# Performance work log

Hardware: AMD Instinct MI355X
Metric: run time of the kernel (lower is better)

## Reference

```python
import jax, jax.numpy as jnp
import numpy as np

N_SAMPLES = 9
N_FEATURES = 8
GRID_DIM = 200
H, W = 512, 512


def _corner_shifts():
    # same ordering as the torch module: i (x) outer, j (y), k (z) inner
    return jnp.array([[i, j, k] for i in (0, 1) for j in (0, 1) for k in (0, 1)], dtype=jnp.int32)


def setup_inputs() -> dict:
    key = jax.random.key(0)
    k1, k2, k3, k4 = jax.random.split(key, 4)
    b = 1
    vpoints = jax.random.uniform(k1, (b, H * W, 3), jnp.float32, 0.0, float(GRID_DIM))
    veye = jax.random.uniform(k2, (b, 3), jnp.float32, -float(GRID_DIM), 0.0)
    depth = jax.random.uniform(k3, (b, H, W), jnp.float32)
    grid = jax.random.normal(k4, (GRID_DIM, GRID_DIM, GRID_DIM, N_FEATURES), jnp.float32)
    empty_value = jnp.zeros((N_FEATURES,), jnp.float32)
    return {"vpoints": vpoints, "veye": veye, "depth": depth, "grid": grid, "empty_value": empty_value}


def _forward(vpoints, veye, depth, grid, empty_value):
    b, h, w = depth.shape
    # --- create_canonical_view: n_samples points along each viewing ray, centered on vpoints ---
    dirs = vpoints - veye[:, None, :]                                   # (b, n, 3)
    dirs = dirs / jnp.linalg.norm(dirs, axis=-1, keepdims=True)
    offs = jnp.arange(N_SAMPLES, dtype=vpoints.dtype) - (N_SAMPLES // 2)
    cv = vpoints[:, :, None, :] + offs[None, None, :, None] * dirs[:, :, None, :]  # (b, n, s, 3)
    points_normalized = cv - (jnp.floor(cv) + 0.5)

    pts = cv.reshape(-1, 3)  # b == 1 (original squeezes the batch dim); N = n*s
    xs, ys, zs, nf = grid.shape
    valid = ((pts[:, 0] >= 0) & (pts[:, 0] < xs)
             & (pts[:, 1] >= 0) & (pts[:, 1] < ys)
             & (pts[:, 2] >= 0) & (pts[:, 2] < zs))

    # replication-pad volume by 1 voxel; coords shifted by +1 into padded frame
    gp = jnp.pad(grid, ((1, 1), (1, 1), (1, 1), (0, 0)), mode="edge")
    p = jnp.where(valid[:, None], pts, 0.0) + 1.0   # invalid points mapped to a safe in-bounds index
    fl = jnp.floor(p)
    df = p - fl                                      # (N, 3) fractional offsets
    base = fl.astype(jnp.int32)
    idx = base[:, None, :] + _corner_shifts()[None]  # (N, 8, 3)

    corners = gp[idx[..., 0], idx[..., 1], idx[..., 2], :]  # (N, 8, nf) gather

    # trilinear weights, ordering matches corner shift ordering (4i + 2j + k)
    wx = jnp.stack([1.0 - df[:, 0], df[:, 0]], axis=1)
    wy = jnp.stack([1.0 - df[:, 1], df[:, 1]], axis=1)
    wz = jnp.stack([1.0 - df[:, 2], df[:, 2]], axis=1)
    wgt = (wx[:, :, None, None] * wy[:, None, :, None] * wz[:, None, None, :]).reshape(-1, 8)

    interp = jnp.einsum("nc,ncf->nf", wgt, corners)              # (N, nf)
    feats = jnp.where(valid[:, None], interp, empty_value[None, :])

    values = feats.reshape(b, h, w, N_SAMPLES * N_FEATURES)
    values = jnp.transpose(values, (0, 3, 1, 2))                 # (b, s*nf, h, w)
    return values, points_normalized, dirs


def reference(vpoints, veye, depth, grid, empty_value):
    return _forward(vpoints, veye, depth, grid, empty_value)
```

## Files before the change

kernel.cpp:

```cpp
#include <hip/hip_runtime.h>

#define HW (512 * 512)
#define GD 200
#define NS 9
#define NF 8
#define NPB 64
#define BT (NPB * NS)

__global__ __launch_bounds__(BT, 5) void fusion_gather_kernel(
    const float* __restrict__ vpoints,
    const float* __restrict__ veye,
    const float* __restrict__ grid,
    const float* __restrict__ empty_value,
    float* __restrict__ out_values,
    float* __restrict__ out_pn,
    float* __restrict__ out_dirs)
{
    __shared__ float pnbuf[NPB * NS * 3];
    __shared__ float dirbuf[NPB * 3];

    int tid = threadIdx.x;
    int s = tid >> 6;
    int i = tid & 63;
    int n0 = blockIdx.x * NPB;
    int n = n0 + i;

    float px = vpoints[n * 3 + 0];
    float py = vpoints[n * 3 + 1];
    float pz = vpoints[n * 3 + 2];
    float ex = veye[0], ey = veye[1], ez = veye[2];

    float dx = px - ex, dy = py - ey, dz = pz - ez;
    float inv = 1.0f / sqrtf(dx * dx + dy * dy + dz * dz);
    dx *= inv; dy *= inv; dz *= inv;

    if (s == 4) {
        dirbuf[i * 3 + 0] = dx;
        dirbuf[i * 3 + 1] = dy;
        dirbuf[i * 3 + 2] = dz;
    }

    float off = (float)(s - NS / 2);
    float cx = px + off * dx;
    float cy = py + off * dy;
    float cz = pz + off * dz;

    pnbuf[i * 27 + s * 3 + 0] = cx - (floorf(cx) + 0.5f);
    pnbuf[i * 27 + s * 3 + 1] = cy - (floorf(cy) + 0.5f);
    pnbuf[i * 27 + s * 3 + 2] = cz - (floorf(cz) + 0.5f);

    bool valid = (cx >= 0.0f) && (cx < (float)GD) &&
                 (cy >= 0.0f) && (cy < (float)GD) &&
                 (cz >= 0.0f) && (cz < (float)GD);

    float p0 = cx + 1.0f, p1 = cy + 1.0f, p2 = cz + 1.0f;
    float f0 = floorf(p0), f1 = floorf(p1), f2 = floorf(p2);
    float d0 = p0 - f0, d1 = p1 - f1, d2 = p2 - f2;
    int bx = (int)f0, by = (int)f1, bz = (int)f2;
    int X0 = min(max(bx - 1, 0), GD - 1), X1 = min(max(bx, 0), GD - 1);
    int Y0 = min(max(by - 1, 0), GD - 1), Y1 = min(max(by, 0), GD - 1);
    int Z0 = min(max(bz - 1, 0), GD - 1), Z1 = min(max(bz, 0), GD - 1);

    const float4* __restrict__ g4 = (const float4*)grid;

    int col[4];
    col[0] = (X0 * GD + Y0) * GD;
    col[1] = (X0 * GD + Y1) * GD;
    col[2] = (X1 * GD + Y0) * GD;
    col[3] = (X1 * GD + Y1) * GD;

    float4 c[16];
#pragma unroll
    for (int q = 0; q < 4; ++q) {
        c[q * 4 + 0] = g4[(size_t)(col[q] + Z0) * 2 + 0];
        c[q * 4 + 1] = g4[(size_t)(col[q] + Z0) * 2 + 1];
        c[q * 4 + 2] = g4[(size_t)(col[q] + Z1) * 2 + 0];
        c[q * 4 + 3] = g4[(size_t)(col[q] + Z1) * 2 + 1];
    }

    float wx0 = 1.0f - d0, wx1 = d0;
    float wy0 = 1.0f - d1, wy1 = d1;
    float wz0 = 1.0f - d2, wz1 = d2;
    float wq[4];
    wq[0] = wx0 * wy0; wq[1] = wx0 * wy1; wq[2] = wx1 * wy0; wq[3] = wx1 * wy1;

    float acc[NF];
#pragma unroll
    for (int f = 0; f < NF; ++f) acc[f] = 0.0f;

#pragma unroll
    for (int q = 0; q < 4; ++q) {
        float w0 = wq[q] * wz0, w1 = wq[q] * wz1;
        acc[0] += w0 * c[q * 4 + 0].x + w1 * c[q * 4 + 2].x;
        acc[1] += w0 * c[q * 4 + 0].y + w1 * c[q * 4 + 2].y;
        acc[2] += w0 * c[q * 4 + 0].z + w1 * c[q * 4 + 2].z;
        acc[3] += w0 * c[q * 4 + 0].w + w1 * c[q * 4 + 2].w;
        acc[4] += w0 * c[q * 4 + 1].x + w1 * c[q * 4 + 3].x;
        acc[5] += w0 * c[q * 4 + 1].y + w1 * c[q * 4 + 3].y;
        acc[6] += w0 * c[q * 4 + 1].z + w1 * c[q * 4 + 3].z;
        acc[7] += w0 * c[q * 4 + 1].w + w1 * c[q * 4 + 3].w;
    }

    float ev[NF];
#pragma unroll
    for (int f = 0; f < NF; ++f) ev[f] = empty_value[f];

#pragma unroll
    for (int f = 0; f < NF; ++f)
        __builtin_nontemporal_store(valid ? acc[f] : ev[f],
                                    &out_values[(size_t)(s * NF + f) * HW + n]);

    __syncthreads();

    const size_t pn_base = (size_t)n0 * (NS * 3);
#pragma unroll
    for (int k = 0; k < 3; ++k) {
        int idx = tid + k * BT;
        __builtin_nontemporal_store(pnbuf[idx], &out_pn[pn_base + idx]);
    }
    if (tid < NPB * 3)
        __builtin_nontemporal_store(dirbuf[tid], &out_dirs[(size_t)n0 * 3 + tid]);
}

extern "C" void kernel_launch(void* const* d_in, const int* in_sizes, int n_in,
                              void* d_out, int out_size, void* d_ws, size_t ws_size,
                              hipStream_t stream) {
    const float* vpoints = (const float*)d_in[0];
    const float* veye = (const float*)d_in[1];
    const float* grid = (const float*)d_in[3];
    const float* empty_value = (const float*)d_in[4];

    float* out = (float*)d_out;
    float* out_values = out;
    float* out_pn = out + (size_t)NS * NF * HW;
    float* out_dirs = out_pn + (size_t)HW * NS * 3;

    dim3 block(BT);
    dim3 grid_dim(HW / NPB);
    hipLaunchKernelGGL(fusion_gather_kernel, grid_dim, block, 0, stream,
                       vpoints, veye, grid, empty_value,
                       out_values, out_pn, out_dirs);
}
```

Baseline: 172.2 us.

## Remap threads so each ray's samples are adjacent and stage outputs through shared memory

Threads are reassigned so the 9 samples of one ray are consecutive lanes (r = tid/9, s = tid%9), which makes neighbouring lanes hit nearby grid voxels for better gather locality. vpoints are staged through shared memory. The feature outputs go into a padded shared buffer and are written back as coalesced rows. The occupancy hint in launch_bounds is dropped. This adds about 18KB of shared memory per block, which may lower occupancy, and adds an integer division.

Result: faster. 158.1 us (median of 2 runs) (-8.2%).

```diff
diff --git a/kernel.cpp b/kernel.cpp
--- a/kernel.cpp
+++ b/kernel.cpp
@@ -7,7 +7,7 @@
 #define NPB 64
 #define BT (NPB * NS)
 
-__global__ __launch_bounds__(BT, 5) void fusion_gather_kernel(
+__global__ __launch_bounds__(BT) void fusion_gather_kernel(
     const float* __restrict__ vpoints,
     const float* __restrict__ veye,
     const float* __restrict__ grid,
@@ -16,28 +16,33 @@
     float* __restrict__ out_pn,
     float* __restrict__ out_dirs)
 {
+    __shared__ float vp[NPB * 3];
     __shared__ float pnbuf[NPB * NS * 3];
     __shared__ float dirbuf[NPB * 3];
+    __shared__ float vbuf[NS * NF * 65];
 
     int tid = threadIdx.x;
-    int s = tid >> 6;
-    int i = tid & 63;
     int n0 = blockIdx.x * NPB;
-    int n = n0 + i;
 
-    float px = vpoints[n * 3 + 0];
-    float py = vpoints[n * 3 + 1];
-    float pz = vpoints[n * 3 + 2];
+    if (tid < NPB * 3) vp[tid] = vpoints[(size_t)n0 * 3 + tid];
+    __syncthreads();
+
+    int r = tid / NS;
+    int s = tid - r * NS;
+
+    float px = vp[r * 3 + 0];
+    float py = vp[r * 3 + 1];
+    float pz = vp[r * 3 + 2];
     float ex = veye[0], ey = veye[1], ez = veye[2];
 
     float dx = px - ex, dy = py - ey, dz = pz - ez;
     float inv = 1.0f / sqrtf(dx * dx + dy * dy + dz * dz);
     dx *= inv; dy *= inv; dz *= inv;
 
-    if (s == 4) {
-        dirbuf[i * 3 + 0] = dx;
-        dirbuf[i * 3 + 1] = dy;
-        dirbuf[i * 3 + 2] = dz;
+    if (s == 0) {
+        dirbuf[r * 3 + 0] = dx;
+        dirbuf[r * 3 + 1] = dy;
+        dirbuf[r * 3 + 2] = dz;
     }
 
     float off = (float)(s - NS / 2);
@@ -45,9 +50,9 @@
     float cy = py + off * dy;
     float cz = pz + off * dz;
 
-    pnbuf[i * 27 + s * 3 + 0] = cx - (floorf(cx) + 0.5f);
-    pnbuf[i * 27 + s * 3 + 1] = cy - (floorf(cy) + 0.5f);
-    pnbuf[i * 27 + s * 3 + 2] = cz - (floorf(cz) + 0.5f);
+    pnbuf[r * 27 + s * 3 + 0] = cx - (floorf(cx) + 0.5f);
+    pnbuf[r * 27 + s * 3 + 1] = cy - (floorf(cy) + 0.5f);
+    pnbuf[r * 27 + s * 3 + 2] = cz - (floorf(cz) + 0.5f);
 
     bool valid = (cx >= 0.0f) && (cx < (float)GD) &&
                  (cy >= 0.0f) && (cy < (float)GD) &&
@@ -107,11 +112,20 @@
 
 #pragma unroll
     for (int f = 0; f < NF; ++f)
-        __builtin_nontemporal_store(valid ? acc[f] : ev[f],
-                                    &out_values[(size_t)(s * NF + f) * HW + n]);
+        vbuf[(s * NF + f) * 65 + r] = valid ? acc[f] : ev[f];
 
     __syncthreads();
 
+    {
+        int col_ = tid & 63;
+        int w = tid >> 6;
+#pragma unroll
+        for (int k = 0; k < 8; ++k) {
+            int row = w + k * NS;
+            __builtin_nontemporal_store(vbuf[row * 65 + col_],
+                                        &out_values[(size_t)row * HW + n0 + col_]);
+        }
+    }
     const size_t pn_base = (size_t)n0 * (NS * 3);
 #pragma unroll
     for (int k = 0; k < 3; ++k) {
```

## Map each ray's nine samples onto adjacent lanes and stage value writes through shared memory

Applied to the files above, without the earlier changes.

Threads are remapped so the nine samples of a ray sit on consecutive lanes of a wave (7 rays per wave, 28 rays per 256-thread block) instead of one sample index per wave. Interpolated values are staged in a padded shared buffer and written out cooperatively per feature row. The goal is to improve locality of the grid gathers, since samples of one ray touch nearby voxels, while keeping the output writes contiguous. In exchange, one lane per wave sits idle, each block writes only 28-float row segments, and there is extra LDS traffic plus a partial tail block.

Result: no change. 171.4 us (-0.5%).

```diff
diff --git a/kernel.cpp b/kernel.cpp
--- a/kernel.cpp
+++ b/kernel.cpp
@@ -4,10 +4,11 @@
 #define GD 200
 #define NS 9
 #define NF 8
-#define NPB 64
-#define BT (NPB * NS)
+#define NPB 28
+#define BT 256
+#define P 29
 
-__global__ __launch_bounds__(BT, 5) void fusion_gather_kernel(
+__global__ __launch_bounds__(BT) void fusion_gather_kernel(
     const float* __restrict__ vpoints,
     const float* __restrict__ veye,
     const float* __restrict__ grid,
@@ -16,109 +17,127 @@
     float* __restrict__ out_pn,
     float* __restrict__ out_dirs)
 {
-    __shared__ float pnbuf[NPB * NS * 3];
+    __shared__ float vbuf[NS * NF * P];
+    __shared__ float pnbuf[NPB * 27];
     __shared__ float dirbuf[NPB * 3];
 
     int tid = threadIdx.x;
-    int s = tid >> 6;
-    int i = tid & 63;
+    int w = tid >> 6;
+    int l = tid & 63;
     int n0 = blockIdx.x * NPB;
-    int n = n0 + i;
+    int nvalid = min(NPB, HW - n0);
 
-    float px = vpoints[n * 3 + 0];
-    float py = vpoints[n * 3 + 1];
-    float pz = vpoints[n * 3 + 2];
-    float ex = veye[0], ey = veye[1], ez = veye[2];
+    if (l < 63) {
+        int r = l / 9;
+        int s = l - r * 9;
+        int lr = w * 7 + r;
+        if (lr < nvalid) {
+            int n = n0 + lr;
 
-    float dx = px - ex, dy = py - ey, dz = pz - ez;
-    float inv = 1.0f / sqrtf(dx * dx + dy * dy + dz * dz);
-    dx *= inv; dy *= inv; dz *= inv;
+            float px = vpoints[n * 3 + 0];
+            float py = vpoints[n * 3 + 1];
+            float pz = vpoints[n * 3 + 2];
+            float ex = veye[0], ey = veye[1], ez = veye[2];
 
-    if (s == 4) {
-        dirbuf[i * 3 + 0] = dx;
-        dirbuf[i * 3 + 1] = dy;
-        dirbuf[i * 3 + 2] = dz;
-    }
+            float dx = px - ex, dy = py - ey, dz = pz - ez;
+            float inv = 1.0f / sqrtf(dx * dx + dy * dy + dz * dz);
+            dx *= inv; dy *= inv; dz *= inv;
 
-    float off = (float)(s - NS / 2);
-    float cx = px + off * dx;
-    float cy = py + off * dy;
-    float cz = pz + off * dz;
+            if (s == 0) {
+                dirbuf[lr * 3 + 0] = dx;
+                dirbuf[lr * 3 + 1] = dy;
+                dirbuf[lr * 3 + 2] = dz;
+            }
 
-    pnbuf[i * 27 + s * 3 + 0] = cx - (floorf(cx) + 0.5f);
-    pnbuf[i * 27 + s * 3 + 1] = cy - (floorf(cy) + 0.5f);
-    pnbuf[i * 27 + s * 3 + 2] = cz - (floorf(cz) + 0.5f);
+            float off = (float)(s - NS / 2);
+            float cx = px + off * dx;
+            float cy = py + off * dy;
+            float cz = pz + off * dz;
 
-    bool valid = (cx >= 0.0f) && (cx < (float)GD) &&
-                 (cy >= 0.0f) && (cy < (float)GD) &&
-                 (cz >= 0.0f) && (cz < (float)GD);
+            pnbuf[lr * 27 + s * 3 + 0] = cx - (floorf(cx) + 0.5f);
+            pnbuf[lr * 27 + s * 3 + 1] = cy - (floorf(cy) + 0.5f);
+            pnbuf[lr * 27 + s * 3 + 2] = cz - (floorf(cz) + 0.5f);
 
-    float p0 = cx + 1.0f, p1 = cy + 1.0f, p2 = cz + 1.0f;
-    float f0 = floorf(p0), f1 = floorf(p1), f2 = floorf(p2);
-    float d0 = p0 - f0, d1 = p1 - f1, d2 = p2 - f2;
-    int bx = (int)f0, by = (int)f1, bz = (int)f2;
-    int X0 = min(max(bx - 1, 0), GD - 1), X1 = min(max(bx, 0), GD - 1);
-    int Y0 = min(max(by - 1, 0), GD - 1), Y1 = min(max(by, 0), GD - 1);
-    int Z0 = min(max(bz - 1, 0), GD - 1), Z1 = min(max(bz, 0), GD - 1);
+            bool valid = (cx >= 0.0f) && (cx < (float)GD) &&
+                         (cy >= 0.0f) && (cy < (float)GD) &&
+                         (cz >= 0.0f) && (cz < (float)GD);
 
-    const float4* __restrict__ g4 = (const float4*)grid;
+            float p0 = cx + 1.0f, p1 = cy + 1.0f, p2 = cz + 1.0f;
+            float f0 = floorf(p0), f1 = floorf(p1), f2 = floorf(p2);
+            float d0 = p0 - f0, d1 = p1 - f1, d2 = p2 - f2;
+            int bx = (int)f0, by = (int)f1, bz = (int)f2;
+            int X0 = min(max(bx - 1, 0), GD - 1), X1 = min(max(bx, 0), GD - 1);
+            int Y0 = min(max(by - 1, 0), GD - 1), Y1 = min(max(by, 0), GD - 1);
+            int Z0 = min(max(bz - 1, 0), GD - 1), Z1 = min(max(bz, 0), GD - 1);
 
-    int col[4];
-    col[0] = (X0 * GD + Y0) * GD;
-    col[1] = (X0 * GD + Y1) * GD;
-    col[2] = (X1 * GD + Y0) * GD;
-    col[3] = (X1 * GD + Y1) * GD;
+            const float4* __restrict__ g4 = (const float4*)grid;
 
-    float4 c[16];
+            int col[4];
+            col[0] = (X0 * GD + Y0) * GD;
+            col[1] = (X0 * GD + Y1) * GD;
+            col[2] = (X1 * GD + Y0) * GD;
+            col[3] = (X1 * GD + Y1) * GD;
+
+            float4 c[16];
 #pragma unroll
-    for (int q = 0; q < 4; ++q) {
-        c[q * 4 + 0] = g4[(size_t)(col[q] + Z0) * 2 + 0];
-        c[q * 4 + 1] = g4[(size_t)(col[q] + Z0) * 2 + 1];
-        c[q * 4 + 2] = g4[(size_t)(col[q] + Z1) * 2 + 0];
-        c[q * 4 + 3] = g4[(size_t)(col[q] + Z1) * 2 + 1];
-    }
+            for (int q = 0; q < 4; ++q) {
+                c[q * 4 + 0] = g4[(size_t)(col[q] + Z0) * 2 + 0];
+                c[q * 4 + 1] = g4[(size_t)(col[q] + Z0) * 2 + 1];
+                c[q * 4 + 2] = g4[(size_t)(col[q] + Z1) * 2 + 0];
+                c[q * 4 + 3] = g4[(size_t)(col[q] + Z1) * 2 + 1];
+            }
 
-    float wx0 = 1.0f - d0, wx1 = d0;
-    float wy0 = 1.0f - d1, wy1 = d1;
-    float wz0 = 1.0f - d2, wz1 = d2;
-    float wq[4];
-    wq[0] = wx0 * wy0; wq[1] = wx0 * wy1; wq[2] = wx1 * wy0; wq[3] = wx1 * wy1;
+            float wx0 = 1.0f - d0, wy0 = 1.0f - d1, wz0 = 1.0f - d2;
+            float wq[4] = {wx0 * wy0, wx0 * d1, d0 * wy0, d0 * d1};
 
-    float acc[NF];
+            float acc[NF];
 #pragma unroll
-    for (int f = 0; f < NF; ++f) acc[f] = 0.0f;
+            for (int f = 0; f < NF; ++f) acc[f] = 0.0f;
 
 #pragma unroll
-    for (int q = 0; q < 4; ++q) {
-        float w0 = wq[q] * wz0, w1 = wq[q] * wz1;
-        acc[0] += w0 * c[q * 4 + 0].x + w1 * c[q * 4 + 2].x;
-        acc[1] += w0 * c[q * 4 + 0].y + w1 * c[q * 4 + 2].y;
-        acc[2] += w0 * c[q * 4 + 0].z + w1 * c[q * 4 + 2].z;
-        acc[3] += w0 * c[q * 4 + 0].w + w1 * c[q * 4 + 2].w;
-        acc[4] += w0 * c[q * 4 + 1].x + w1 * c[q * 4 + 3].x;
-        acc[5] += w0 * c[q * 4 + 1].y + w1 * c[q * 4 + 3].y;
-        acc[6] += w0 * c[q * 4 + 1].z + w1 * c[q * 4 + 3].z;
-        acc[7] += w0 * c[q * 4 + 1].w + w1 * c[q * 4 + 3].w;
-    }
+            for (int q = 0; q < 4; ++q) {
+                float w0 = wq[q] * wz0, w1 = wq[q] * d2;
+                acc[0] += w0 * c[q * 4 + 0].x + w1 * c[q * 4 + 2].x;
+                acc[1] += w0 * c[q * 4 + 0].y + w1 * c[q * 4 + 2].y;
+                acc[2] += w0 * c[q * 4 + 0].z + w1 * c[q * 4 + 2].z;
+                acc[3] += w0 * c[q * 4 + 0].w + w1 * c[q * 4 + 2].w;
+                acc[4] += w0 * c[q * 4 + 1].x + w1 * c[q * 4 + 3].x;
+                acc[5] += w0 * c[q * 4 + 1].y + w1 * c[q * 4 + 3].y;
+                acc[6] += w0 * c[q * 4 + 1].z + w1 * c[q * 4 + 3].z;
+                acc[7] += w0 * c[q * 4 + 1].w + w1 * c[q * 4 + 3].w;
+            }
 
-    float ev[NF];
+            float ev[NF];
 #pragma unroll
-    for (int f = 0; f < NF; ++f) ev[f] = empty_value[f];
+            for (int f = 0; f < NF; ++f) ev[f] = empty_value[f];
 
 #pragma unroll
-    for (int f = 0; f < NF; ++f)
-        __builtin_nontemporal_store(valid ? acc[f] : ev[f],
-                                    &out_values[(size_t)(s * NF + f) * HW + n]);
+            for (int f = 0; f < NF; ++f)
+                vbuf[(s * NF + f) * P + lr] = valid ? acc[f] : ev[f];
+        }
+    }
 
     __syncthreads();
 
-    const size_t pn_base = (size_t)n0 * (NS * 3);
 #pragma unroll
-    for (int k = 0; k < 3; ++k) {
-        int idx = tid + k * BT;
-        __builtin_nontemporal_store(pnbuf[idx], &out_pn[pn_base + idx]);
+    for (int j = 0; j < 8; ++j) {
+        int idx = tid + j * BT;
+        if (idx < NS * NF * NPB) {
+            int row = idx / NPB;
+            int col = idx - row * NPB;
+            if (col < nvalid)
+                __builtin_nontemporal_store(vbuf[row * P + col],
+                                            &out_values[(size_t)row * HW + n0 + col]);
+        }
     }
-    if (tid < NPB * 3)
+    const size_t pn_base = (size_t)n0 * 27;
+#pragma unroll
+    for (int j = 0; j < 3; ++j) {
+        int idx = tid + j * BT;
+        if (idx < nvalid * 27)
+            __builtin_nontemporal_store(pnbuf[idx], &out_pn[pn_base + idx]);
+    }
+    if (tid < nvalid * 3)
         __builtin_nontemporal_store(dirbuf[tid], &out_dirs[(size_t)n0 * 3 + tid]);
 }
 
@@ -136,7 +155,7 @@
     float* out_dirs = out_pn + (size_t)HW * NS * 3;
 
     dim3 block(BT);
-    dim3 grid_dim(HW / NPB);
+    dim3 grid_dim((HW + NPB - 1) / NPB);
     hipLaunchKernelGGL(fusion_gather_kernel, grid_dim, block, 0, stream,
                        vpoints, veye, grid, empty_value,
                        out_values, out_pn, out_dirs);
```
